# Kernel optimization log

Measured on AMD Instinct MI355X. Metric: run time of the kernel, lower is better.

The kernel has to match this reference:

```python
import jax, jax.numpy as jnp
import numpy as np

B, L = 64, 1024
ENC, DEC, ATT = 2048, 512, 512


def setup_inputs() -> dict:
    key = jax.random.key(0)
    ks = jax.random.split(key, 8)
    s_enc = 1.0 / np.sqrt(ENC)
    s_dec = 1.0 / np.sqrt(DEC)
    s_att = 1.0 / np.sqrt(ATT)
    return {
        "encoder_out": jax.random.normal(ks[0], (B, L, ENC), jnp.float32),
        "decoder_hidden": jax.random.normal(ks[1], (B, DEC), jnp.float32),
        "W_enc": jax.random.uniform(ks[2], (ENC, ATT), jnp.float32, -s_enc, s_enc),
        "b_enc": jax.random.uniform(ks[3], (ATT,), jnp.float32, -s_enc, s_enc),
        "W_dec": jax.random.uniform(ks[4], (DEC, ATT), jnp.float32, -s_dec, s_dec),
        "b_dec": jax.random.uniform(ks[5], (ATT,), jnp.float32, -s_dec, s_dec),
        "W_full": jax.random.uniform(ks[6], (ATT, 1), jnp.float32, -s_att, s_att),
        "b_full": jax.random.uniform(ks[7], (1,), jnp.float32, -s_att, s_att),
    }


def reference(encoder_out, decoder_hidden, W_enc, b_enc, W_dec, b_dec, W_full, b_full):
    # att1: (B, L, ATT)
    att1 = jnp.einsum('ble,ea->bla', encoder_out, W_enc) + b_enc
    # att2: (B, ATT)
    att2 = decoder_hidden @ W_dec + b_dec
    score = jax.nn.relu(att1 + att2[:, None, :])            # (B, L, ATT)
    logits = (score @ W_full).squeeze(-1) + b_full[0]       # (B, L)
    att = jax.nn.softmax(logits, axis=1)                    # (B, L)
    context_vector = jnp.einsum('bl,ble->be', att, encoder_out)  # (B, ENC)
    return (context_vector, att)
```

## Files before the change

kernel.cpp:

```cpp
#include <hip/hip_runtime.h>

typedef unsigned short u16;
typedef unsigned int u32;
typedef __bf16 bf16x8 __attribute__((ext_vector_type(8)));
typedef float f32x4 __attribute__((ext_vector_type(4)));

#define BM 128
#define BN 128
#define BK 64
#define BKB 32
#define KDIM 2048
#define NDIM 512
#define MDIM 65536
#define LROW 40

typedef __attribute__((address_space(3))) void lds_void;
typedef const __attribute__((address_space(1))) void glb_void;
#define LOAD_LDS16(g, l) \
  __builtin_amdgcn_global_load_lds((glb_void*)(g), (lds_void*)(l), 16, 0, 0)

__device__ __forceinline__ u16 f2bf(float f) {
  u32 u = __float_as_uint(f);
  u += 0x7FFFu + ((u >> 16) & 1u);
  return (u16)(u >> 16);
}

__global__ __launch_bounds__(256) void wenc_t(const float* __restrict__ W, u16* __restrict__ WT) {
  const int n = blockIdx.x;
  for (int k = threadIdx.x; k < KDIM; k += 256)
    WT[n * KDIM + k] = f2bf(W[k * NDIM + n]);
}

__global__ __launch_bounds__(256) void wenc_pack(const float* __restrict__ W,
                                                 u16* __restrict__ Bp) {
  const int t = blockIdx.x * 256 + threadIdx.x;
  const int lane = t & 63;
  const int h = (t >> 6) & 1;
  const int kk = (t >> 7) & 31;
  const int g16 = t >> 12;
  const int l15 = lane & 15, quad = lane >> 4;
  const int n = g16 * 16 + l15;
  const int k0 = kk * 64 + h * 32 + quad * 8;
  u16 o[8];
#pragma unroll
  for (int j = 0; j < 8; j++) o[j] = f2bf(W[(size_t)(k0 + j) * NDIM + n]);
  *(uint4*)(Bp + (size_t)t * 8) = *(const uint4*)o;
}

__global__ __launch_bounds__(256) void att2_kernel(const float* __restrict__ dec,
                                                   const float* __restrict__ Wd,
                                                   const float* __restrict__ bd,
                                                   const float* __restrict__ be,
                                                   float* __restrict__ att2) {
  const int idx = blockIdx.x * 256 + threadIdx.x;
  const int b = idx >> 9, a = idx & 511;
  float s = bd[a] + be[a];
  const float* dp = dec + b * 512;
#pragma unroll 8
  for (int d = 0; d < 512; d++) s += dp[d] * Wd[d * NDIM + a];
  att2[idx] = s;
}

__global__ __launch_bounds__(256) void enc_to_bf16(const float* __restrict__ src,
                                                   u16* __restrict__ dst) {
  const size_t tidg = (size_t)blockIdx.x * 256 + threadIdx.x;
#pragma unroll
  for (int it = 0; it < 8; it++) {
    const size_t base = ((size_t)it * 16777216) + tidg * 8;
    const float4 x = *(const float4*)(src + base);
    const float4 y = *(const float4*)(src + base + 4);
    uint4 o;
    o.x = f2bf(x.x) | ((u32)f2bf(x.y) << 16);
    o.y = f2bf(x.z) | ((u32)f2bf(x.w) << 16);
    o.z = f2bf(y.x) | ((u32)f2bf(y.y) << 16);
    o.w = f2bf(y.z) | ((u32)f2bf(y.w) << 16);
    *(uint4*)(dst + base) = o;
  }
}

__global__ __launch_bounds__(256) void gemm_logits_a(const u16* __restrict__ A,
                                                     const u16* __restrict__ Bp,
                                                     const float* __restrict__ att2,
                                                     const float* __restrict__ Wfull,
                                                     float* __restrict__ partial) {
  __shared__ u16 As[BM * BK];
  __shared__ float lds_logit[BM];

  const int tid = threadIdx.x;
  const int flat = blockIdx.x;
  const int x = flat & 7;
  const int nb = (flat >> 3) & 3;
  const int mb = ((flat >> 5) << 3) + x;
  const int rowBase = mb * BM;
  const int colBase = nb * BN;
  const int b = rowBase >> 10;

  if (tid < BM) lds_logit[tid] = 0.f;

  const int lane = tid & 63, wid = tid >> 6;
  const int wr = (wid >> 1) * 64, wc = (wid & 1) * 64;
  const int quad = lane >> 4, l15 = lane & 15;

  float att2v[4], wfv[4];
#pragma unroll
  for (int j = 0; j < 4; j++) {
    const int g = colBase + wc + j * 16 + l15;
    att2v[j] = att2[b * NDIM + g];
    wfv[j] = Wfull[g];
  }

  const u16* AgS[4];
  u16* AsD[4];
#pragma unroll
  for (int s = 0; s < 4; s++) {
    const int c = s * 256 + tid;
    const int r = c >> 3;
    const int kc = (c & 7) ^ (r & 7);
    AgS[s] = A + (size_t)(rowBase + r) * KDIM + kc * 8;
    AsD[s] = &As[c * 8];
  }

  const int g16_0 = (colBase + wc) >> 4;
  const uint4* BpV = (const uint4*)Bp;

  f32x4 acc[4][4];
#pragma unroll
  for (int i = 0; i < 4; i++)
#pragma unroll
    for (int j = 0; j < 4; j++) acc[i][j] = (f32x4)0.f;

  for (int kk = 0; kk < KDIM / BK; kk++) {
    const int ko = kk * BK;
    __syncthreads();
#pragma unroll
    for (int s = 0; s < 4; s++) LOAD_LDS16(AgS[s] + ko, AsD[s]);
    uint4 braw[2][4];
#pragma unroll
    for (int h = 0; h < 2; h++)
#pragma unroll
      for (int j = 0; j < 4; j++)
        braw[h][j] = BpV[(g16_0 + j) * 4096 + kk * 128 + h * 64 + lane];
    __syncthreads();

    bf16x8 afr[2][4];
#pragma unroll
    for (int h = 0; h < 2; h++)
#pragma unroll
      for (int i = 0; i < 4; i++) {
        const int m = wr + i * 16 + l15;
        afr[h][i] = *(const bf16x8*)&As[m * BK + ((((h << 2) | quad) ^ (l15 & 7)) << 3)];
      }
#pragma unroll
    for (int h = 0; h < 2; h++)
#pragma unroll
      for (int i = 0; i < 4; i++)
#pragma unroll
        for (int j = 0; j < 4; j++)
          acc[i][j] = __builtin_amdgcn_mfma_f32_16x16x32_bf16(
              afr[h][i], *(const bf16x8*)&braw[h][j], acc[i][j], 0, 0, 0);
  }

#pragma unroll
  for (int i = 0; i < 4; i++) {
#pragma unroll
    for (int r = 0; r < 4; r++) {
      float s = 0.f;
#pragma unroll
      for (int j = 0; j < 4; j++) {
        float v = acc[i][j][r] + att2v[j];
        v = v > 0.f ? v : 0.f;
        s += v * wfv[j];
      }
      s += __shfl_xor(s, 1, 64);
      s += __shfl_xor(s, 2, 64);
      s += __shfl_xor(s, 4, 64);
      s += __shfl_xor(s, 8, 64);
      if (l15 == 0) atomicAdd(&lds_logit[wr + i * 16 + quad * 4 + r], s);
    }
  }
  __syncthreads();
  if (tid < BM) partial[(size_t)nb * MDIM + rowBase + tid] = lds_logit[tid];
}

__global__ __launch_bounds__(256, 2) void gemm_logits_b(const float* __restrict__ enc,
                                                        const u16* __restrict__ WT,
                                                        const float* __restrict__ att2,
                                                        const float* __restrict__ Wfull,
                                                        float* __restrict__ partial) {
  __shared__ u16 As[BM * LROW];
  __shared__ u16 Bs[BN * LROW];
  __shared__ float lds_logit[BM];

  const int tid = threadIdx.x;
  const int flat = blockIdx.x;
  const int x = flat & 7;
  const int nb = (flat >> 3) & 3;
  const int mb = ((flat >> 5) << 3) + x;
  const int rowBase = mb * BM, colBase = nb * BN;
  const int b = rowBase >> 10;
  if (tid < BM) lds_logit[tid] = 0.f;
  const int lane = tid & 63, wid = tid >> 6;
  const int wr = (wid >> 1) * 64, wc = (wid & 1) * 64;
  const int quad = lane >> 4, l15 = lane & 15;

  float att2v[4], wfv[4];
#pragma unroll
  for (int j = 0; j < 4; j++) {
    const int g = colBase + wc + j * 16 + l15;
    att2v[j] = att2[b * NDIM + g];
    wfv[j] = Wfull[g];
  }
  const int srow = tid >> 1, shalf = tid & 1;
  const float* Ag = enc + (size_t)(rowBase + srow) * KDIM + shalf * 16;
  const u16* Bg = WT + (size_t)(colBase + srow) * KDIM + shalf * 16;

  f32x4 acc[4][4];
#pragma unroll
  for (int i = 0; i < 4; i++)
#pragma unroll
    for (int j = 0; j < 4; j++) acc[i][j] = (f32x4)0.f;

  float4 a0, a1, a2, a3;
  uint4 bb0, bb1;
  auto loadA = [&](int k0) {
    const float* p = Ag + k0;
    a0 = *(const float4*)(p);
    a1 = *(const float4*)(p + 4);
    a2 = *(const float4*)(p + 8);
    a3 = *(const float4*)(p + 12);
  };
  auto loadB = [&](int k0) {
    const u16* p = Bg + k0;
    bb0 = *(const uint4*)(p);
    bb1 = *(const uint4*)(p + 8);
  };
  loadA(0);
  loadB(0);
  u16* AsW = &As[srow * LROW + shalf * 16];
  u16* BsW = &Bs[srow * LROW + shalf * 16];
  const u16* aRd = &As[(wr + l15) * LROW + quad * 8];
  const u16* bRd = &Bs[(wc + l15) * LROW + quad * 8];

  for (int kk = 0; kk < KDIM / BKB; kk++) {
    __syncthreads();
    u32 w0 = f2bf(a0.x) | ((u32)f2bf(a0.y) << 16);
    u32 w1 = f2bf(a0.z) | ((u32)f2bf(a0.w) << 16);
    u32 w2 = f2bf(a1.x) | ((u32)f2bf(a1.y) << 16);
    u32 w3 = f2bf(a1.z) | ((u32)f2bf(a1.w) << 16);
    u32 w4 = f2bf(a2.x) | ((u32)f2bf(a2.y) << 16);
    u32 w5 = f2bf(a2.z) | ((u32)f2bf(a2.w) << 16);
    u32 w6 = f2bf(a3.x) | ((u32)f2bf(a3.y) << 16);
    u32 w7 = f2bf(a3.z) | ((u32)f2bf(a3.w) << 16);
    *(uint4*)AsW = make_uint4(w0, w1, w2, w3);
    *(uint4*)(AsW + 8) = make_uint4(w4, w5, w6, w7);
    *(uint4*)BsW = bb0;
    *(uint4*)(BsW + 8) = bb1;
    __syncthreads();
    if (kk + 1 < KDIM / BKB) {
      loadA((kk + 1) * BKB);
      loadB((kk + 1) * BKB);
    }
    bf16x8 afr[4], bfr[4];
#pragma unroll
    for (int i = 0; i < 4; i++) afr[i] = *(const bf16x8*)(aRd + i * 16 * LROW);
#pragma unroll
    for (int j = 0; j < 4; j++) bfr[j] = *(const bf16x8*)(bRd + j * 16 * LROW);
#pragma unroll
    for (int i = 0; i < 4; i++)
#pragma unroll
      for (int j = 0; j < 4; j++)
        acc[i][j] = __builtin_amdgcn_mfma_f32_16x16x32_bf16(afr[i], bfr[j], acc[i][j], 0, 0, 0);
  }
#pragma unroll
  for (int i = 0; i < 4; i++) {
#pragma unroll
    for (int r = 0; r < 4; r++) {
      float s = 0.f;
#pragma unroll
      for (int j = 0; j < 4; j++) {
        float v = acc[i][j][r] + att2v[j];
        v = v > 0.f ? v : 0.f;
        s += v * wfv[j];
      }
      s += __shfl_xor(s, 1, 64);
      s += __shfl_xor(s, 2, 64);
      s += __shfl_xor(s, 4, 64);
      s += __shfl_xor(s, 8, 64);
      if (l15 == 0) atomicAdd(&lds_logit[wr + i * 16 + quad * 4 + r], s);
    }
  }
  __syncthreads();
  if (tid < BM) partial[(size_t)nb * MDIM + rowBase + tid] = lds_logit[tid];
}

__global__ __launch_bounds__(256) void softmax_kernel(const float* __restrict__ partial,
                                                      const float* __restrict__ b_full,
                                                      float* __restrict__ att_out) {
  const int b = blockIdx.x, tid = threadIdx.x;
  const int lane = tid & 63, wid = tid >> 6;
  __shared__ float red[4];
  const float bf0 = b_full[0];
  float v[4];
  float m = -3.4e38f;
#pragma unroll
  for (int c = 0; c < 4; c++) {
    const int idx = b * 1024 + c * 256 + tid;
    float s = partial[idx] + partial[MDIM + idx] + partial[2 * MDIM + idx] +
              partial[3 * MDIM + idx] + bf0;
    v[c] = s;
    m = fmaxf(m, s);
  }
#pragma unroll
  for (int o = 1; o < 64; o <<= 1) m = fmaxf(m, __shfl_xor(m, o, 64));
  if (lane == 0) red[wid] = m;
  __syncthreads();
  m = fmaxf(fmaxf(red[0], red[1]), fmaxf(red[2], red[3]));
  __syncthreads();
  float s = 0.f;
#pragma unroll
  for (int c = 0; c < 4; c++) {
    v[c] = expf(v[c] - m);
    s += v[c];
  }
#pragma unroll
  for (int o = 1; o < 64; o <<= 1) s += __shfl_xor(s, o, 64);
  if (lane == 0) red[wid] = s;
  __syncthreads();
  const float inv = 1.0f / (red[0] + red[1] + red[2] + red[3]);
#pragma unroll
  for (int c = 0; c < 4; c++) att_out[b * 1024 + c * 256 + tid] = v[c] * inv;
}

__global__ __launch_bounds__(256) void ctx_partial_a(const float* __restrict__ enc,
                                                     const float* __restrict__ att,
                                                     float* __restrict__ ctxp) {
  const int x = blockIdx.x;
  const int lc = x & 15, ec = (x >> 4) & 1, b = x >> 5;
  const int tid = threadIdx.x;
  __shared__ float aw[64];
  if (tid < 64) aw[tid] = att[b * 1024 + lc * 64 + tid];
  __syncthreads();
  const int e0 = ec * 1024 + tid * 4;
  float4 acc = {0.f, 0.f, 0.f, 0.f};
  const float* base = enc + (size_t)b * 1024 * 2048 + (size_t)(lc * 64) * 2048 + e0;
#pragma unroll 16
  for (int l = 0; l < 64; l++) {
    const float w = aw[l];
    const float4 v = *(const float4*)(base + (size_t)l * 2048);
    acc.x += w * v.x;
    acc.y += w * v.y;
    acc.z += w * v.z;
    acc.w += w * v.w;
  }
  *(float4*)(ctxp + (size_t)lc * 131072 + b * 2048 + e0) = acc;
}

__global__ __launch_bounds__(256) void ctx_reduce_a(const float* __restrict__ ctxp,
                                                    float* __restrict__ out) {
  const int i = blockIdx.x * 256 + threadIdx.x;
  float s = 0.f;
#pragma unroll
  for (int lc = 0; lc < 16; lc++) s += ctxp[(size_t)lc * 131072 + i];
  out[i] = s;
}

__global__ __launch_bounds__(256) void ctx_partial_b(const float* __restrict__ enc,
                                                     const float* __restrict__ att,
                                                     float* __restrict__ ctxp) {
  const int x = blockIdx.x;
  const int lc = x & 3, ec = (x >> 2) & 1, b = x >> 3;
  const int tid = threadIdx.x;
  __shared__ float aw[256];
  aw[tid] = att[b * 1024 + lc * 256 + tid];
  __syncthreads();
  const int e0 = ec * 1024 + tid * 4;
  float4 acc = {0.f, 0.f, 0.f, 0.f};
  const float* base = enc + (size_t)b * 1024 * 2048 + (size_t)(lc * 256) * 2048 + e0;
#pragma unroll 4
  for (int l = 0; l < 256; l++) {
    const float w = aw[l];
    const float4 v = *(const float4*)(base + (size_t)l * 2048);
    acc.x += w * v.x;
    acc.y += w * v.y;
    acc.z += w * v.z;
    acc.w += w * v.w;
  }
  *(float4*)(ctxp + (size_t)lc * 131072 + b * 2048 + e0) = acc;
}

__global__ __launch_bounds__(256) void ctx_reduce_b(const float* __restrict__ ctxp,
                                                    float* __restrict__ out) {
  const int i = blockIdx.x * 256 + threadIdx.x;
  out[i] = ctxp[i] + ctxp[131072 + i] + ctxp[262144 + i] + ctxp[393216 + i];
}

extern "C" void kernel_launch(void* const* d_in, const int* in_sizes, int n_in,
                              void* d_out, int out_size, void* d_ws, size_t ws_size,
                              hipStream_t stream) {
  const float* enc    = (const float*)d_in[0];
  const float* dec    = (const float*)d_in[1];
  const float* W_enc  = (const float*)d_in[2];
  const float* b_enc  = (const float*)d_in[3];
  const float* W_dec  = (const float*)d_in[4];
  const float* b_dec  = (const float*)d_in[5];
  const float* W_full = (const float*)d_in[6];
  const float* b_full = (const float*)d_in[7];
  float* out = (float*)d_out;
  char* ws = (char*)d_ws;

  const size_t MB = 1u << 20;
  const size_t needA = 256 * MB + 2 * MB + MB + MB;

  if (ws_size >= needA) {
    u16* encb = (u16*)ws;
    float* ctxp = (float*)ws;
    u16* Bp = (u16*)(ws + 256 * MB);
    float* att2 = (float*)(ws + 258 * MB);
    float* partial = (float*)(ws + 258 * MB + 128 * 1024);

    wenc_pack<<<512, 256, 0, stream>>>(W_enc, Bp);
    att2_kernel<<<128, 256, 0, stream>>>(dec, W_dec, b_dec, b_enc, att2);
    enc_to_bf16<<<8192, 256, 0, stream>>>(enc, encb);
    gemm_logits_a<<<2048, 256, 0, stream>>>(encb, Bp, att2, W_full, partial);
    softmax_kernel<<<64, 256, 0, stream>>>(partial, b_full, out + 131072);
    ctx_partial_a<<<2048, 256, 0, stream>>>(enc, out + 131072, ctxp);
    ctx_reduce_a<<<512, 256, 0, stream>>>(ctxp, out);
  } else {
    u16* WT = (u16*)ws;
    float* ctxp = (float*)ws;
    float* att2 = (float*)(ws + 2 * MB);
    float* partial = (float*)(ws + 2 * MB + 128 * 1024);

    wenc_t<<<512, 256, 0, stream>>>(W_enc, WT);
    att2_kernel<<<128, 256, 0, stream>>>(dec, W_dec, b_dec, b_enc, att2);
    gemm_logits_b<<<2048, 256, 0, stream>>>(enc, WT, att2, W_full, partial);
    softmax_kernel<<<64, 256, 0, stream>>>(partial, b_full, out + 131072);
    ctx_partial_b<<<512, 256, 0, stream>>>(enc, out + 131072, ctxp);
    ctx_reduce_b<<<512, 256, 0, stream>>>(ctxp, out);
  }
}
```

Before: 1.077 ms.

## Fuse fp32-to-bf16 encoder conversion into GEMM A-tile loads with register prefetch

```diff
diff --git a/kernel.cpp b/kernel.cpp
--- a/kernel.cpp
+++ b/kernel.cpp
@@ -13,11 +13,6 @@
 #define NDIM 512
 #define MDIM 65536
 #define LROW 40
-
-typedef __attribute__((address_space(3))) void lds_void;
-typedef const __attribute__((address_space(1))) void glb_void;
-#define LOAD_LDS16(g, l) \
-  __builtin_amdgcn_global_load_lds((glb_void*)(g), (lds_void*)(l), 16, 0, 0)
 
 __device__ __forceinline__ u16 f2bf(float f) {
   u32 u = __float_as_uint(f);
@@ -61,24 +56,7 @@
   att2[idx] = s;
 }
 
-__global__ __launch_bounds__(256) void enc_to_bf16(const float* __restrict__ src,
-                                                   u16* __restrict__ dst) {
-  const size_t tidg = (size_t)blockIdx.x * 256 + threadIdx.x;
-#pragma unroll
-  for (int it = 0; it < 8; it++) {
-    const size_t base = ((size_t)it * 16777216) + tidg * 8;
-    const float4 x = *(const float4*)(src + base);
-    const float4 y = *(const float4*)(src + base + 4);
-    uint4 o;
-    o.x = f2bf(x.x) | ((u32)f2bf(x.y) << 16);
-    o.y = f2bf(x.z) | ((u32)f2bf(x.w) << 16);
-    o.z = f2bf(y.x) | ((u32)f2bf(y.y) << 16);
-    o.w = f2bf(y.z) | ((u32)f2bf(y.w) << 16);
-    *(uint4*)(dst + base) = o;
-  }
-}
-
-__global__ __launch_bounds__(256) void gemm_logits_a(const u16* __restrict__ A,
+__global__ __launch_bounds__(256) void gemm_logits_f(const float* __restrict__ A,
                                                      const u16* __restrict__ Bp,
                                                      const float* __restrict__ att2,
                                                      const float* __restrict__ Wfull,
@@ -109,14 +87,14 @@
     wfv[j] = Wfull[g];
   }
 
-  const u16* AgS[4];
+  const float* AgF[4];
   u16* AsD[4];
 #pragma unroll
   for (int s = 0; s < 4; s++) {
     const int c = s * 256 + tid;
     const int r = c >> 3;
-    const int kc = (c & 7) ^ (r & 7);
-    AgS[s] = A + (size_t)(rowBase + r) * KDIM + kc * 8;
+    const int g = (c & 7) ^ (r & 7);
+    AgF[s] = A + (size_t)(rowBase + r) * KDIM + g * 8;
     AsD[s] = &As[c * 8];
   }
 
@@ -129,18 +107,35 @@
 #pragma unroll
     for (int j = 0; j < 4; j++) acc[i][j] = (f32x4)0.f;
 
+  float4 pa0[4], pa1[4];
+  auto loadA = [&](int ko) {
+#pragma unroll
+    for (int s = 0; s < 4; s++) {
+      pa0[s] = *(const float4*)(AgF[s] + ko);
+      pa1[s] = *(const float4*)(AgF[s] + ko + 4);
+    }
+  };
+  loadA(0);
+
   for (int kk = 0; kk < KDIM / BK; kk++) {
-    const int ko = kk * BK;
     __syncthreads();
-#pragma unroll
-    for (int s = 0; s < 4; s++) LOAD_LDS16(AgS[s] + ko, AsD[s]);
     uint4 braw[2][4];
 #pragma unroll
     for (int h = 0; h < 2; h++)
 #pragma unroll
       for (int j = 0; j < 4; j++)
         braw[h][j] = BpV[(g16_0 + j) * 4096 + kk * 128 + h * 64 + lane];
+#pragma unroll
+    for (int s = 0; s < 4; s++) {
+      uint4 o;
+      o.x = f2bf(pa0[s].x) | ((u32)f2bf(pa0[s].y) << 16);
+      o.y = f2bf(pa0[s].z) | ((u32)f2bf(pa0[s].w) << 16);
+      o.z = f2bf(pa1[s].x) | ((u32)f2bf(pa1[s].y) << 16);
+      o.w = f2bf(pa1[s].z) | ((u32)f2bf(pa1[s].w) << 16);
+      *(uint4*)AsD[s] = o;
+    }
     __syncthreads();
+    if (kk + 1 < KDIM / BK) loadA((kk + 1) * BK);
 
     bf16x8 afr[2][4];
 #pragma unroll
@@ -409,19 +404,17 @@
   char* ws = (char*)d_ws;
 
   const size_t MB = 1u << 20;
-  const size_t needA = 256 * MB + 2 * MB + MB + MB;
-
-  if (ws_size >= needA) {
-    u16* encb = (u16*)ws;
-    float* ctxp = (float*)ws;
-    u16* Bp = (u16*)(ws + 256 * MB);
-    float* att2 = (float*)(ws + 258 * MB);
-    float* partial = (float*)(ws + 258 * MB + 128 * 1024);
+  const size_t needF = 16 * MB;
+
+  if (ws_size >= needF) {
+    u16* Bp = (u16*)ws;
+    float* att2 = (float*)(ws + 2 * MB);
+    float* partial = (float*)(ws + 2 * MB + 128 * 1024);
+    float* ctxp = (float*)(ws + 4 * MB);
 
     wenc_pack<<<512, 256, 0, stream>>>(W_enc, Bp);
     att2_kernel<<<128, 256, 0, stream>>>(dec, W_dec, b_dec, b_enc, att2);
-    enc_to_bf16<<<8192, 256, 0, stream>>>(enc, encb);
-    gemm_logits_a<<<2048, 256, 0, stream>>>(encb, Bp, att2, W_full, partial);
+    gemm_logits_f<<<2048, 256, 0, stream>>>(enc, Bp, att2, W_full, partial);
     softmax_kernel<<<64, 256, 0, stream>>>(partial, b_full, out + 131072);
     ctx_partial_a<<<2048, 256, 0, stream>>>(enc, out + 131072, ctxp);
     ctx_reduce_a<<<512, 256, 0, stream>>>(ctxp, out);
```

Result: faster. 961.2 us (-10.7%).
